# Performance work log

Measured on AMD Instinct MI355X. Metric: run time of the kernel, lower is better.

The kernel has to match this reference:

```python
import jax, jax.numpy as jnp
import numpy as np

NUM = 128
IN_F = NUM * NUM        # 16384
HID = NUM * 3           # 384 (infl_ratio = 3)
OUT = 10
BATCH = 8192
BN_EPS = 1e-5


def sign_ste(t):
    # Deterministic sign binarization with straight-through gradient,
    # matching the torch .data/.org mutation trick.
    return t + jax.lax.stop_gradient(jnp.sign(t) - t)


def setup_inputs() -> dict:
    key = jax.random.key(0)
    k_x, k_w1, k_w4 = jax.random.split(key, 3)
    x = jax.random.normal(k_x, (BATCH, IN_F), dtype=jnp.float32)
    W1 = jax.random.normal(k_w1, (HID, IN_F), dtype=jnp.float32) * 0.02
    W4 = jax.random.normal(k_w4, (OUT, HID), dtype=jnp.float32) * 0.02
    gamma = jnp.ones((HID,), dtype=jnp.float32)
    beta = jnp.zeros((HID,), dtype=jnp.float32)
    return {"x": x, "W1": W1, "gamma": gamma, "beta": beta, "W4": W4}


def reference(x, W1, gamma, beta, W4):
    x = x.reshape(-1, IN_F)
    # fc1: in_features (16384) != 784, so the hard-coded check binarizes the input too
    xb = sign_ste(x)
    h = jnp.einsum('bk,hk->bh', xb, sign_ste(W1))  # [B, HID]
    # BatchNorm1d, training mode: batch stats, biased variance
    mean = jnp.mean(h, axis=0)
    var = jnp.mean(jnp.square(h - mean), axis=0)
    h = (h - mean) * jax.lax.rsqrt(var + BN_EPS) * gamma + beta
    # Hardtanh
    h = jnp.clip(h, -1.0, 1.0)
    # fc4: input size 384 != 784 -> binarize activations, binarize weights
    out = jnp.einsum('bh,oh->bo', sign_ste(h), sign_ste(W4))  # [B, 10]
    return out
```

## Files before the change

kernel.cpp:

```cpp
#include <hip/hip_runtime.h>
#include <cstdint>
#include <cstddef>


typedef float v4f __attribute__((ext_vector_type(4)));
typedef long long v2l __attribute__((ext_vector_type(2)));

#define BATCH   8192
#define KDIM    16384
#define HID     384
#define OUT_F   10
#define BK      64
#define MT      32
#define SPLITK  4
#define KPB     (KDIM / SPLITK)
#define NIT     (KPB / BK)
#define WCHUNK  (HID * BK)

#define WS_W1C   0
#define WS_H     (6291456)
#define WS_GSUM  (WS_H + 12582912)
#define WS_GSQ   (WS_GSUM + 3072)
#define WS_MEAN  (WS_GSQ + 3072)
#define WS_COEF  (WS_MEAN + 3072)
#define WS_SW4   (WS_COEF + 3072)

__device__ __forceinline__ uint32_t pack_sign4(v4f v) {
    uint32_t p = 0;
#pragma unroll
    for (int i = 0; i < 4; ++i) {
        uint32_t u = __float_as_uint(v[i]);
        uint32_t b = ((u & 0x7fffffffu) == 0u) ? 0u : (0x38u | ((u >> 24) & 0x80u));
        p |= b << (8 * i);
    }
    return p;
}

__global__ void prep_w1(const float* __restrict__ W1, uint8_t* __restrict__ W1c) {
    size_t e = ((size_t)blockIdx.x * blockDim.x + threadIdx.x) * 4;
    int c   = (int)(e >> 14);
    int k   = (int)(e & 16383);
    int it  = k >> 6;
    int kin = k & 63;
    int s   = kin >> 5;
    int q   = (kin >> 3) & 3;
    int j   = kin & 7;
    v4f w = *(const v4f*)(W1 + e);
    uint32_t p = pack_sign4(w);
    *(uint32_t*)(W1c + (((size_t)it * HID + c) * 4 + q) * 16 + s * 8 + j) = p;
}

__global__ __launch_bounds__(256, 4) void gemm1(const float* __restrict__ x,
                                                const uint8_t* __restrict__ W1c,
                                                float* __restrict__ h) {
    __shared__ __align__(16) uint8_t Xs[2][MT * 72];

    const int t    = threadIdx.x;
    const int wave = t >> 6;
    const int lane = t & 63;
    const int q    = lane >> 4;
    const int l15  = lane & 15;
    const int kblk = blockIdx.x & (SPLITK - 1);
    const int m0   = (blockIdx.x >> 2) * MT;

    const int xrow = t >> 3;
    const int xk8  = (t & 7) * 8;
    const float* xp = x + (size_t)(m0 + xrow) * KDIM + (size_t)kblk * KPB + xk8;

    const uint8_t* wp = W1c + (size_t)kblk * ((size_t)NIT * WCHUNK)
                      + (((size_t)(wave * 96 + l15)) * 4 + q) * 16;

    v4f acc[2][6];
#pragma unroll
    for (int mt = 0; mt < 2; ++mt)
#pragma unroll
        for (int nt = 0; nt < 6; ++nt)
            acc[mt][nt] = v4f{0.f, 0.f, 0.f, 0.f};

    v2l wc[6];
    {
#pragma unroll
        for (int nt = 0; nt < 6; ++nt)
            wc[nt] = *(const v2l*)(wp + nt * 1024);
        v4f xa = *(const v4f*)(xp);
        v4f xb = *(const v4f*)(xp + 4);
        uint2 pk; pk.x = pack_sign4(xa); pk.y = pack_sign4(xb);
        *(uint2*)&Xs[0][xrow * 72 + xk8] = pk;
    }
    __syncthreads();

#pragma unroll 2
    for (int it = 0; it < NIT; ++it) {
        const int cur = it & 1;
        const bool more = (it + 1) < NIT;
        v2l wn[6];
        v4f xa, xb;
        if (more) {
            const uint8_t* wpn = wp + (size_t)(it + 1) * WCHUNK;
#pragma unroll
            for (int nt = 0; nt < 6; ++nt)
                wn[nt] = *(const v2l*)(wpn + nt * 1024);
            xa = *(const v4f*)(xp + (size_t)(it + 1) * BK);
            xb = *(const v4f*)(xp + (size_t)(it + 1) * BK + 4);
        }

#pragma unroll
        for (int s = 0; s < 2; ++s) {
            long long a[2];
#pragma unroll
            for (int mt = 0; mt < 2; ++mt)
                a[mt] = *(const long long*)&Xs[cur][(mt * 16 + l15) * 72 + s * 32 + q * 8];
#pragma unroll
            for (int nt = 0; nt < 6; ++nt)
#pragma unroll
                for (int mt = 0; mt < 2; ++mt)
                    acc[mt][nt] = __builtin_amdgcn_mfma_f32_16x16x32_fp8_fp8(
                        a[mt], wc[nt][s], acc[mt][nt], 0, 0, 0);
        }

        if (more) {
            uint2 pk; pk.x = pack_sign4(xa); pk.y = pack_sign4(xb);
            *(uint2*)&Xs[cur ^ 1][xrow * 72 + xk8] = pk;
#pragma unroll
            for (int nt = 0; nt < 6; ++nt) wc[nt] = wn[nt];
        }
        __syncthreads();
    }

#pragma unroll
    for (int nt = 0; nt < 6; ++nt) {
        const int col = wave * 96 + nt * 16 + l15;
#pragma unroll
        for (int mt = 0; mt < 2; ++mt)
#pragma unroll
            for (int r = 0; r < 4; ++r)
                atomicAdd(&h[(size_t)(m0 + mt * 16 + q * 4 + r) * HID + col],
                          acc[mt][nt][r]);
    }
}

__global__ void colstats(const float* __restrict__ h,
                         double* __restrict__ gsum, double* __restrict__ gsq) {
    int j  = threadIdx.x;
    int r0 = blockIdx.x * 16;
    double s = 0.0, sq = 0.0;
#pragma unroll
    for (int r = 0; r < 16; ++r) {
        double v = (double)h[(size_t)(r0 + r) * HID + j];
        s += v;
        sq += v * v;
    }
    atomicAdd(&gsum[j], s);
    atomicAdd(&gsq[j], sq);
}

__global__ void finalize(const double* __restrict__ gsum, const double* __restrict__ gsq,
                         const float* __restrict__ gamma, const float* __restrict__ W4,
                         double* __restrict__ meanArr, double* __restrict__ coefArr,
                         float* __restrict__ sW4) {
    int j = threadIdx.x;
    double mean = gsum[j] * (1.0 / (double)BATCH);
    double var  = gsq[j] * (1.0 / (double)BATCH) - mean * mean;
    meanArr[j] = mean;
    coefArr[j] = (double)gamma[j] / sqrt(var + 1e-5);
#pragma unroll
    for (int o = 0; o < OUT_F; ++o) {
        float w = W4[o * HID + j];
        sW4[o * HID + j] = (w > 0.f) ? 1.f : ((w < 0.f) ? -1.f : 0.f);
    }
}

__global__ __launch_bounds__(256) void head(const float* __restrict__ h,
                                            const double* __restrict__ meanArr,
                                            const double* __restrict__ coefArr,
                                            const float* __restrict__ beta,
                                            const float* __restrict__ sW4,
                                            float* __restrict__ out) {
    int wave = threadIdx.x >> 6;
    int lane = threadIdx.x & 63;
    int b = blockIdx.x * 4 + wave;
    float a[OUT_F];
#pragma unroll
    for (int o = 0; o < OUT_F; ++o) a[o] = 0.f;
#pragma unroll
    for (int i = 0; i < 6; ++i) {
        int j = lane + i * 64;
        double v = ((double)h[(size_t)b * HID + j] - meanArr[j]) * coefArr[j]
                 + (double)beta[j];
        float s = (v > 0.0) ? 1.f : ((v < 0.0) ? -1.f : 0.f);
#pragma unroll
        for (int o = 0; o < OUT_F; ++o) a[o] += s * sW4[o * HID + j];
    }
#pragma unroll
    for (int o = 0; o < OUT_F; ++o) {
#pragma unroll
        for (int off = 32; off > 0; off >>= 1) a[o] += __shfl_down(a[o], off);
    }
    if (lane == 0) {
#pragma unroll
        for (int o = 0; o < OUT_F; ++o) out[(size_t)b * OUT_F + o] = a[o];
    }
}

extern "C" void kernel_launch(void* const* d_in, const int* in_sizes, int n_in,
                              void* d_out, int out_size, void* d_ws, size_t ws_size,
                              hipStream_t stream) {
    const float* x     = (const float*)d_in[0];
    const float* W1    = (const float*)d_in[1];
    const float* gamma = (const float*)d_in[2];
    const float* beta  = (const float*)d_in[3];
    const float* W4    = (const float*)d_in[4];
    float* out = (float*)d_out;

    uint8_t* ws = (uint8_t*)d_ws;
    uint8_t* W1c     = ws + WS_W1C;
    float*   h       = (float*)(ws + WS_H);
    double*  gsum    = (double*)(ws + WS_GSUM);
    double*  gsq     = (double*)(ws + WS_GSQ);
    double*  meanArr = (double*)(ws + WS_MEAN);
    double*  coefArr = (double*)(ws + WS_COEF);
    float*   sW4     = (float*)(ws + WS_SW4);

    prep_w1<<<6144, 256, 0, stream>>>(W1, W1c);
    hipMemsetAsync(ws + WS_H, 0, 12582912 + 2 * HID * sizeof(double), stream);
    gemm1<<<(BATCH / MT) * SPLITK, 256, 0, stream>>>(x, W1c, h);
    colstats<<<BATCH / 16, HID, 0, stream>>>(h, gsum, gsq);
    finalize<<<1, HID, 0, stream>>>(gsum, gsq, gamma, W4, meanArr, coefArr, sW4);
    head<<<BATCH / 4, 256, 0, stream>>>(h, meanArr, coefArr, beta, sW4, out);
}
```

Before: 799.8 us.

## Pre-binarize x into MFMA-ready fp8 layout and drop LDS staging in gemm1

Adds a prep_x kernel that converts x to fp8 sign values once, stored in a tiled layout that matches the MFMA operand order. gemm1 then loads these packed operands straight into registers, with no LDS double buffer and no per-iteration barriers. Before, each of the four blocks sharing an M tile converted its own k-slice of x inside the GEMM. The cost is an extra kernel pass that reads all of x (512MB fp32) and writes 128MB of fp8, which gemm1 then reads back.

New measurement: 898.0 us. 1.12x slower.

```diff
diff --git a/kernel.cpp b/kernel.cpp
--- a/kernel.cpp
+++ b/kernel.cpp
@@ -24,6 +24,7 @@
 #define WS_MEAN  (WS_GSQ + 3072)
 #define WS_COEF  (WS_MEAN + 3072)
 #define WS_SW4   (WS_COEF + 3072)
+#define WS_XB    (WS_SW4 + 15360)
 
 __device__ __forceinline__ uint32_t pack_sign4(v4f v) {
     uint32_t p = 0;
@@ -50,11 +51,28 @@
     *(uint32_t*)(W1c + (((size_t)it * HID + c) * 4 + q) * 16 + s * 8 + j) = p;
 }
 
-__global__ __launch_bounds__(256, 4) void gemm1(const float* __restrict__ x,
+__global__ void prep_x(const float* __restrict__ x, uint8_t* __restrict__ xb) {
+    size_t g = (size_t)blockIdx.x * blockDim.x + threadIdx.x;
+    int k8  = ((int)g & 7) * 8;
+    int r   = ((int)(g >> 3)) & 31;
+    int itg = ((int)(g >> 8)) & 255;
+    int mb  = (int)(g >> 16);
+    int row = mb * 32 + r;
+    int k   = itg * 64 + k8;
+    const float* px = x + (size_t)row * KDIM + k;
+    v4f a = *(const v4f*)px;
+    v4f b = *(const v4f*)(px + 4);
+    int s = k8 >> 5;
+    int q = (k8 >> 3) & 3;
+    uint2 p;
+    p.x = pack_sign4(a);
+    p.y = pack_sign4(b);
+    *(uint2*)(xb + (((size_t)mb * 256 + itg) * 32 + r) * 64 + q * 16 + s * 8) = p;
+}
+
+__global__ __launch_bounds__(256, 4) void gemm1(const uint8_t* __restrict__ xb,
                                                 const uint8_t* __restrict__ W1c,
                                                 float* __restrict__ h) {
-    __shared__ __align__(16) uint8_t Xs[2][MT * 72];
-
     const int t    = threadIdx.x;
     const int wave = t >> 6;
     const int lane = t & 63;
@@ -63,10 +81,8 @@
     const int kblk = blockIdx.x & (SPLITK - 1);
     const int m0   = (blockIdx.x >> 2) * MT;
 
-    const int xrow = t >> 3;
-    const int xk8  = (t & 7) * 8;
-    const float* xp = x + (size_t)(m0 + xrow) * KDIM + (size_t)kblk * KPB + xk8;
-
+    const uint8_t* xp = xb + ((size_t)(blockIdx.x >> 2) * 256 + (size_t)kblk * NIT) * 2048
+                      + (size_t)l15 * 64 + q * 16;
     const uint8_t* wp = W1c + (size_t)kblk * ((size_t)NIT * WCHUNK)
                       + (((size_t)(wave * 96 + l15)) * 4 + q) * 16;
 
@@ -77,55 +93,41 @@
         for (int nt = 0; nt < 6; ++nt)
             acc[mt][nt] = v4f{0.f, 0.f, 0.f, 0.f};
 
-    v2l wc[6];
-    {
-#pragma unroll
-        for (int nt = 0; nt < 6; ++nt)
-            wc[nt] = *(const v2l*)(wp + nt * 1024);
-        v4f xa = *(const v4f*)(xp);
-        v4f xb = *(const v4f*)(xp + 4);
-        uint2 pk; pk.x = pack_sign4(xa); pk.y = pack_sign4(xb);
-        *(uint2*)&Xs[0][xrow * 72 + xk8] = pk;
-    }
-    __syncthreads();
+    v2l wc[6], xc[2];
+#pragma unroll
+    for (int nt = 0; nt < 6; ++nt) wc[nt] = *(const v2l*)(wp + nt * 1024);
+    xc[0] = *(const v2l*)(xp);
+    xc[1] = *(const v2l*)(xp + 1024);
+
+#define COMPUTE_STEP                                                         \
+    _Pragma("unroll")                                                        \
+    for (int s = 0; s < 2; ++s)                                              \
+        _Pragma("unroll")                                                    \
+        for (int nt = 0; nt < 6; ++nt)                                       \
+            _Pragma("unroll")                                                \
+            for (int mt = 0; mt < 2; ++mt)                                   \
+                acc[mt][nt] = __builtin_amdgcn_mfma_f32_16x16x32_fp8_fp8(    \
+                    xc[mt][s], wc[nt][s], acc[mt][nt], 0, 0, 0);
 
 #pragma unroll 2
-    for (int it = 0; it < NIT; ++it) {
-        const int cur = it & 1;
-        const bool more = (it + 1) < NIT;
-        v2l wn[6];
-        v4f xa, xb;
-        if (more) {
-            const uint8_t* wpn = wp + (size_t)(it + 1) * WCHUNK;
-#pragma unroll
-            for (int nt = 0; nt < 6; ++nt)
-                wn[nt] = *(const v2l*)(wpn + nt * 1024);
-            xa = *(const v4f*)(xp + (size_t)(it + 1) * BK);
-            xb = *(const v4f*)(xp + (size_t)(it + 1) * BK + 4);
-        }
-
-#pragma unroll
-        for (int s = 0; s < 2; ++s) {
-            long long a[2];
-#pragma unroll
-            for (int mt = 0; mt < 2; ++mt)
-                a[mt] = *(const long long*)&Xs[cur][(mt * 16 + l15) * 72 + s * 32 + q * 8];
-#pragma unroll
-            for (int nt = 0; nt < 6; ++nt)
-#pragma unroll
-                for (int mt = 0; mt < 2; ++mt)
-                    acc[mt][nt] = __builtin_amdgcn_mfma_f32_16x16x32_fp8_fp8(
-                        a[mt], wc[nt][s], acc[mt][nt], 0, 0, 0);
-        }
-
-        if (more) {
-            uint2 pk; pk.x = pack_sign4(xa); pk.y = pack_sign4(xb);
-            *(uint2*)&Xs[cur ^ 1][xrow * 72 + xk8] = pk;
-#pragma unroll
-            for (int nt = 0; nt < 6; ++nt) wc[nt] = wn[nt];
-        }
-        __syncthreads();
-    }
+    for (int it = 0; it < NIT - 1; ++it) {
+        v2l wn[6], xn[2];
+        const uint8_t* wpn = wp + (size_t)(it + 1) * WCHUNK;
+        const uint8_t* xpn = xp + (size_t)(it + 1) * 2048;
+#pragma unroll
+        for (int nt = 0; nt < 6; ++nt) wn[nt] = *(const v2l*)(wpn + nt * 1024);
+        xn[0] = *(const v2l*)(xpn);
+        xn[1] = *(const v2l*)(xpn + 1024);
+
+        COMPUTE_STEP
+
+#pragma unroll
+        for (int nt = 0; nt < 6; ++nt) wc[nt] = wn[nt];
+        xc[0] = xn[0];
+        xc[1] = xn[1];
+    }
+    COMPUTE_STEP
+#undef COMPUTE_STEP
 
 #pragma unroll
     for (int nt = 0; nt < 6; ++nt) {
@@ -220,10 +222,12 @@
     double*  meanArr = (double*)(ws + WS_MEAN);
     double*  coefArr = (double*)(ws + WS_COEF);
     float*   sW4     = (float*)(ws + WS_SW4);
+    uint8_t* xb      = ws + WS_XB;
 
     prep_w1<<<6144, 256, 0, stream>>>(W1, W1c);
+    prep_x<<<65536, 256, 0, stream>>>(x, xb);
     hipMemsetAsync(ws + WS_H, 0, 12582912 + 2 * HID * sizeof(double), stream);
-    gemm1<<<(BATCH / MT) * SPLITK, 256, 0, stream>>>(x, W1c, h);
+    gemm1<<<(BATCH / MT) * SPLITK, 256, 0, stream>>>(xb, W1c, h);
     colstats<<<BATCH / 16, HID, 0, stream>>>(h, gsum, gsq);
     finalize<<<1, HID, 0, stream>>>(gsum, gsq, gamma, W4, meanArr, coefArr, sW4);
     head<<<BATCH / 4, 256, 0, stream>>>(h, meanArr, coefArr, beta, sW4, out);
```
